# Kernel optimization log

Hardware: AMD Instinct MI355X
Metric: run time of the kernel (lower is better)

Reference implementation:

```python
import jax, jax.numpy as jnp
import numpy as np

I, H, O = 3, 16, 5
B, S = 4096, 512


def setup_inputs() -> dict:
    key = jax.random.key(0)
    ks = jax.random.split(key, 4)
    scale = 0.1  # xavier gain=0.1 ballpark; exact init irrelevant for correctness baseline
    return {
        "x": jax.random.normal(ks[0], (B, S, I), dtype=jnp.float32),
        "W_ih": jax.random.normal(ks[1], (4 * H, I), dtype=jnp.float32) * scale,
        "W_hh": jax.random.normal(ks[2], (4 * H, H), dtype=jnp.float32) * scale,
        "b_ih": jnp.zeros((4 * H,), dtype=jnp.float32),
        "b_hh": jnp.zeros((4 * H,), dtype=jnp.float32),
        "W_lin": jax.random.normal(ks[3], (O, H), dtype=jnp.float32) * scale,
        "b_lin": jnp.zeros((O,), dtype=jnp.float32),
    }


def _lstm(x, W_ih, W_hh, b_ih, b_hh):
    # Precompute input contribution for all timesteps: [B, S, 4H]
    xg = jnp.einsum('bsi,gi->bsg', x, W_ih) + b_ih + b_hh
    xg = jnp.swapaxes(xg, 0, 1)  # [S, B, 4H] for scan
    h0 = jnp.zeros((x.shape[0], H), dtype=x.dtype)
    c0 = jnp.zeros_like(h0)

    def step(carry, xt):
        h, c = carry
        gates = xt + h @ W_hh.T  # [B, 4H]
        i, f, g, o = jnp.split(gates, 4, axis=-1)  # PyTorch gate order i,f,g,o
        i = jax.nn.sigmoid(i)
        f = jax.nn.sigmoid(f)
        g = jnp.tanh(g)
        o = jax.nn.sigmoid(o)
        c = f * c + i * g
        h = o * jnp.tanh(c)
        return (h, c), h

    _, hs = jax.lax.scan(step, (h0, c0), xg)
    return jnp.swapaxes(hs, 0, 1)  # [B, S, H]


def reference(x, W_ih, W_hh, b_ih, b_hh, W_lin, b_lin):
    out1 = _lstm(x, W_ih, W_hh, b_ih, b_hh)            # [B, S, H]
    out = jnp.einsum('bsh,oh->bso', out1, W_lin) + b_lin  # [B, S, O]
    return jnp.clip(out, -10.0, 10.0)
```

## Files before the change

kernel.cpp:

```cpp
#include <hip/hip_runtime.h>


#define TS 512
#define LOG2E 1.44269504088896340736f

typedef float f32x2 __attribute__((ext_vector_type(2)));

#define BCAST(K) hbr[K] = __int_as_float( \
    __builtin_amdgcn_update_dpp(0, hvi, 0x150 + (K), 0xf, 0xf, true))
#define BCAST_ALL() \
  BCAST(0); BCAST(1); BCAST(2); BCAST(3); BCAST(4); BCAST(5); BCAST(6); BCAST(7); \
  BCAST(8); BCAST(9); BCAST(10); BCAST(11); BCAST(12); BCAST(13); BCAST(14); BCAST(15)

__global__ __launch_bounds__(256, 1)
void lstm_enc_kernel(const float* __restrict__ x,
                     const float* __restrict__ W_ih,
                     const float* __restrict__ W_hh,
                     const float* __restrict__ b_ih,
                     const float* __restrict__ b_hh,
                     const float* __restrict__ W_lin,
                     const float* __restrict__ b_lin,
                     float* __restrict__ out) {
  const int tid = threadIdx.x;
  const int j = tid & 15;
  const int batch = blockIdx.x * 16 + (tid >> 4);
  const int jo = (j < 5) ? j : 0;

  f32x2 wif[16], wgo[16];
  float wl[16];
#pragma unroll
  for (int k = 0; k < 16; ++k) {
    wif[k] = f32x2{W_hh[(j     ) * 16 + k] * LOG2E,
                   W_hh[(j + 16) * 16 + k] * LOG2E};
    wgo[k] = f32x2{W_hh[(j + 32) * 16 + k] * (2.0f * LOG2E),
                   W_hh[(j + 48) * 16 + k] * LOG2E};
    wl[k]  = W_lin[jo * 16 + k];
  }
  f32x2 xif[3], xgo[3];
#pragma unroll
  for (int i = 0; i < 3; ++i) {
    xif[i] = f32x2{W_ih[(j     ) * 3 + i] * LOG2E,
                   W_ih[(j + 16) * 3 + i] * LOG2E};
    xgo[i] = f32x2{W_ih[(j + 32) * 3 + i] * (2.0f * LOG2E),
                   W_ih[(j + 48) * 3 + i] * LOG2E};
  }
  const f32x2 bif = f32x2{(b_ih[j     ] + b_hh[j     ]) * LOG2E,
                          (b_ih[j + 16] + b_hh[j + 16]) * LOG2E};
  const f32x2 bgo = f32x2{(b_ih[j + 32] + b_hh[j + 32]) * (2.0f * LOG2E),
                          (b_ih[j + 48] + b_hh[j + 48]) * LOG2E};
  const float bl = b_lin[jo];

  const float* __restrict__ xb = x + (size_t)batch * (TS * 3);
  float* __restrict__ ob = out + (size_t)batch * (TS * 5) + j;

  float h = 0.0f, c = 0.0f;
  float x0 = xb[0], x1 = xb[1], x2 = xb[2];

  for (int t = 0; t < TS; ++t) {
    const int tn = (t + 1) & (TS - 1);
    const float nx0 = xb[tn * 3 + 0];
    const float nx1 = xb[tn * 3 + 1];
    const float nx2 = xb[tn * 3 + 2];

    float hbr[16];
    const int hvi = __float_as_int(h);
    BCAST_ALL();

    f32x2 aif = bif, ago = bgo;
    float oa = bl;
    aif = f32x2{x0, x0} * xif[0] + aif;
    aif = f32x2{x1, x1} * xif[1] + aif;
    aif = f32x2{x2, x2} * xif[2] + aif;
    ago = f32x2{x0, x0} * xgo[0] + ago;
    ago = f32x2{x1, x1} * xgo[1] + ago;
    ago = f32x2{x2, x2} * xgo[2] + ago;
#pragma unroll
    for (int k = 0; k < 16; ++k) {
      const float hk = hbr[k];
      const f32x2 h2 = f32x2{hk, hk};
      aif = h2 * wif[k] + aif;
      ago = h2 * wgo[k] + ago;
      oa = fmaf(hk, wl[k], oa);
    }

    if (t > 0 && j < 5) {
      ob[(t - 1) * 5] = fminf(fmaxf(oa, -10.0f), 10.0f);
    }

    const float ig = __builtin_amdgcn_rcpf(1.0f + __builtin_amdgcn_exp2f(-aif.x));
    const float fg = __builtin_amdgcn_rcpf(1.0f + __builtin_amdgcn_exp2f(-aif.y));
    const float gg = fmaf(-2.0f, __builtin_amdgcn_rcpf(1.0f + __builtin_amdgcn_exp2f(ago.x)), 1.0f);
    const float og = __builtin_amdgcn_rcpf(1.0f + __builtin_amdgcn_exp2f(-ago.y));

    c = fmaf(fg, c, ig * gg);
    const float tc = fmaf(-2.0f,
        __builtin_amdgcn_rcpf(1.0f + __builtin_amdgcn_exp2f((2.0f * LOG2E) * c)), 1.0f);
    h = og * tc;

    x0 = nx0; x1 = nx1; x2 = nx2;
  }

  {
    float hbr[16];
    const int hvi = __float_as_int(h);
    BCAST_ALL();
    float oa = bl;
#pragma unroll
    for (int k = 0; k < 16; ++k) oa = fmaf(hbr[k], wl[k], oa);
    if (j < 5) {
      ob[(TS - 1) * 5] = fminf(fmaxf(oa, -10.0f), 10.0f);
    }
  }
}

extern "C" void kernel_launch(void* const* d_in, const int* in_sizes, int n_in,
                              void* d_out, int out_size, void* d_ws, size_t ws_size,
                              hipStream_t stream) {
  const float* x     = (const float*)d_in[0];
  const float* W_ih  = (const float*)d_in[1];
  const float* W_hh  = (const float*)d_in[2];
  const float* b_ih  = (const float*)d_in[3];
  const float* b_hh  = (const float*)d_in[4];
  const float* W_lin = (const float*)d_in[5];
  const float* b_lin = (const float*)d_in[6];
  float* out = (float*)d_out;

  const int B = in_sizes[0] / (TS * 3);
  const int grid = B / 16;
  lstm_enc_kernel<<<grid, 256, 0, stream>>>(x, W_ih, W_hh, b_ih, b_hh, W_lin, b_lin, out);
}
```

Measured before the change: 236.5 us.

## Split LSTM gates across two 16-lane rows and exchange via ds_swizzle

Each batch element now uses 32 lanes instead of 16. One 16-lane row computes the i/f gates and the other the g/o gates, halving the per-lane recurrent FMA work and the transcendentals. The gate results are exchanged with a ds_swizzle, and the accumulation is split into two chains to expose ILP. The grid doubles and launch bounds allow two blocks per CU, trading more threads, redundant cell/h updates and the output dot product on both rows, plus swizzle latency, for a shorter per-step critical path.

```diff
diff --git a/kernel.cpp b/kernel.cpp
--- a/kernel.cpp
+++ b/kernel.cpp
@@ -12,7 +12,9 @@
   BCAST(0); BCAST(1); BCAST(2); BCAST(3); BCAST(4); BCAST(5); BCAST(6); BCAST(7); \
   BCAST(8); BCAST(9); BCAST(10); BCAST(11); BCAST(12); BCAST(13); BCAST(14); BCAST(15)
 
-__global__ __launch_bounds__(256, 1)
+#define SWZ16(vi) __builtin_amdgcn_ds_swizzle((vi), 0x401F)
+
+__global__ __launch_bounds__(256, 2)
 void lstm_enc_kernel(const float* __restrict__ x,
                      const float* __restrict__ W_ih,
                      const float* __restrict__ W_hh,
@@ -23,35 +25,34 @@
                      float* __restrict__ out) {
   const int tid = threadIdx.x;
   const int j = tid & 15;
-  const int batch = blockIdx.x * 16 + (tid >> 4);
+  const bool rowB = (tid & 16) != 0;
+  const int batch = blockIdx.x * 8 + (tid >> 5);
   const int jo = (j < 5) ? j : 0;
 
-  f32x2 wif[16], wgo[16];
+  const int g0 = rowB ? j + 32 : j;
+  const int g1 = rowB ? j + 48 : j + 16;
+  const float s0 = rowB ? 2.0f * LOG2E : -LOG2E;
+  const float s1 = -LOG2E;
+
+  f32x2 wz[16];
   float wl[16];
 #pragma unroll
   for (int k = 0; k < 16; ++k) {
-    wif[k] = f32x2{W_hh[(j     ) * 16 + k] * LOG2E,
-                   W_hh[(j + 16) * 16 + k] * LOG2E};
-    wgo[k] = f32x2{W_hh[(j + 32) * 16 + k] * (2.0f * LOG2E),
-                   W_hh[(j + 48) * 16 + k] * LOG2E};
-    wl[k]  = W_lin[jo * 16 + k];
+    wz[k] = f32x2{W_hh[g0 * 16 + k] * s0, W_hh[g1 * 16 + k] * s1};
+    wl[k] = W_lin[jo * 16 + k];
   }
-  f32x2 xif[3], xgo[3];
+  f32x2 xw[3];
 #pragma unroll
   for (int i = 0; i < 3; ++i) {
-    xif[i] = f32x2{W_ih[(j     ) * 3 + i] * LOG2E,
-                   W_ih[(j + 16) * 3 + i] * LOG2E};
-    xgo[i] = f32x2{W_ih[(j + 32) * 3 + i] * (2.0f * LOG2E),
-                   W_ih[(j + 48) * 3 + i] * LOG2E};
+    xw[i] = f32x2{W_ih[g0 * 3 + i] * s0, W_ih[g1 * 3 + i] * s1};
   }
-  const f32x2 bif = f32x2{(b_ih[j     ] + b_hh[j     ]) * LOG2E,
-                          (b_ih[j + 16] + b_hh[j + 16]) * LOG2E};
-  const f32x2 bgo = f32x2{(b_ih[j + 32] + b_hh[j + 32]) * (2.0f * LOG2E),
-                          (b_ih[j + 48] + b_hh[j + 48]) * LOG2E};
+  const f32x2 bz = f32x2{(b_ih[g0] + b_hh[g0]) * s0,
+                         (b_ih[g1] + b_hh[g1]) * s1};
   const float bl = b_lin[jo];
 
   const float* __restrict__ xb = x + (size_t)batch * (TS * 3);
   float* __restrict__ ob = out + (size_t)batch * (TS * 5) + j;
+  const bool storer = (tid & 31) < 5;
 
   float h = 0.0f, c = 0.0f;
   float x0 = xb[0], x1 = xb[1], x2 = xb[2];
@@ -66,32 +67,35 @@
     const int hvi = __float_as_int(h);
     BCAST_ALL();
 
-    f32x2 aif = bif, ago = bgo;
+    f32x2 za = bz, zb = f32x2{0.0f, 0.0f};
+    za = f32x2{x0, x0} * xw[0] + za;
+    zb = f32x2{x1, x1} * xw[1] + zb;
+    za = f32x2{x2, x2} * xw[2] + za;
+#pragma unroll
+    for (int k = 0; k < 16; k += 2) {
+      za = f32x2{hbr[k], hbr[k]} * wz[k] + za;
+      zb = f32x2{hbr[k + 1], hbr[k + 1]} * wz[k + 1] + zb;
+    }
+    const f32x2 z = za + zb;
+
     float oa = bl;
-    aif = f32x2{x0, x0} * xif[0] + aif;
-    aif = f32x2{x1, x1} * xif[1] + aif;
-    aif = f32x2{x2, x2} * xif[2] + aif;
-    ago = f32x2{x0, x0} * xgo[0] + ago;
-    ago = f32x2{x1, x1} * xgo[1] + ago;
-    ago = f32x2{x2, x2} * xgo[2] + ago;
 #pragma unroll
-    for (int k = 0; k < 16; ++k) {
-      const float hk = hbr[k];
-      const f32x2 h2 = f32x2{hk, hk};
-      aif = h2 * wif[k] + aif;
-      ago = h2 * wgo[k] + ago;
-      oa = fmaf(hk, wl[k], oa);
-    }
-
-    if (t > 0 && j < 5) {
+    for (int k = 0; k < 16; ++k) oa = fmaf(hbr[k], wl[k], oa);
+    if (t > 0 && storer) {
       ob[(t - 1) * 5] = fminf(fmaxf(oa, -10.0f), 10.0f);
     }
 
-    const float ig = __builtin_amdgcn_rcpf(1.0f + __builtin_amdgcn_exp2f(-aif.x));
-    const float fg = __builtin_amdgcn_rcpf(1.0f + __builtin_amdgcn_exp2f(-aif.y));
-    const float gg = fmaf(-2.0f, __builtin_amdgcn_rcpf(1.0f + __builtin_amdgcn_exp2f(ago.x)), 1.0f);
-    const float og = __builtin_amdgcn_rcpf(1.0f + __builtin_amdgcn_exp2f(-ago.y));
+    const float r0 = __builtin_amdgcn_rcpf(1.0f + __builtin_amdgcn_exp2f(z.x));
+    const float r1 = __builtin_amdgcn_rcpf(1.0f + __builtin_amdgcn_exp2f(z.y));
 
+    const float q0 = __int_as_float(SWZ16(__float_as_int(r0)));
+    const float q1 = __int_as_float(SWZ16(__float_as_int(r1)));
+    const float ig = rowB ? q0 : r0;
+    const float fg = rowB ? q1 : r1;
+    const float sg = rowB ? r0 : q0;
+    const float og = rowB ? r1 : q1;
+
+    const float gg = fmaf(-2.0f, sg, 1.0f);
     c = fmaf(fg, c, ig * gg);
     const float tc = fmaf(-2.0f,
         __builtin_amdgcn_rcpf(1.0f + __builtin_amdgcn_exp2f((2.0f * LOG2E) * c)), 1.0f);
@@ -107,7 +111,7 @@
     float oa = bl;
 #pragma unroll
     for (int k = 0; k < 16; ++k) oa = fmaf(hbr[k], wl[k], oa);
-    if (j < 5) {
+    if (storer) {
       ob[(TS - 1) * 5] = fminf(fmaxf(oa, -10.0f), 10.0f);
     }
   }
@@ -126,6 +130,6 @@
   float* out = (float*)d_out;
 
   const int B = in_sizes[0] / (TS * 3);
-  const int grid = B / 16;
+  const int grid = B / 8;
   lstm_enc_kernel<<<grid, 256, 0, stream>>>(x, W_ih, W_hh, b_ih, b_hh, W_lin, b_lin, out);
 }
```

Measured after the change: 267.1 us. 1.13x slower.

## Stage x through LDS in 64-step chunks and split gate accumulators into two chains

Applied to the files above, without the earlier changes.

The 16 lanes of each batch group now cooperatively load 64 timesteps of x with coalesced float4 loads and scatter them into a double-buffered shared-memory tile. Each step then reads its x values from LDS with a two-step lookahead instead of issuing three scalar global loads per timestep. The gate dot products are split into two independent FMA accumulator chains to shorten the dependency chain on the recurrent critical path. This adds LDS traffic and register pressure. There is no barrier between the LDS writes and the reads, which relies on the 16 lanes of a group sharing one wavefront.

```diff
diff --git a/kernel.cpp b/kernel.cpp
--- a/kernel.cpp
+++ b/kernel.cpp
@@ -23,8 +23,12 @@
                      float* __restrict__ out) {
   const int tid = threadIdx.x;
   const int j = tid & 15;
-  const int batch = blockIdx.x * 16 + (tid >> 4);
+  const int g = tid >> 4;
+  const int batch = blockIdx.x * 16 + g;
   const int jo = (j < 5) ? j : 0;
+
+  __shared__ float4 xs[2][64][16];
+  float4* xsf = &xs[0][0][0];
 
   f32x2 wif[16], wgo[16];
   float wl[16];
@@ -36,12 +40,16 @@
                    W_hh[(j + 48) * 16 + k] * LOG2E};
     wl[k]  = W_lin[jo * 16 + k];
   }
-  f32x2 xif[3], xgo[3];
+  f32x2 xw[3];
 #pragma unroll
   for (int i = 0; i < 3; ++i) {
-    xif[i] = f32x2{W_ih[(j     ) * 3 + i] * LOG2E,
-                   W_ih[(j + 16) * 3 + i] * LOG2E};
-    xgo[i] = f32x2{W_ih[(j + 32) * 3 + i] * (2.0f * LOG2E),
+    xw[i] = f32x2{W_ih[(j     ) * 3 + i] * LOG2E,
+                  W_ih[(j + 16) * 3 + i] * LOG2E};
+  }
+  f32x2 xwg[3];
+#pragma unroll
+  for (int i = 0; i < 3; ++i) {
+    xwg[i] = f32x2{W_ih[(j + 32) * 3 + i] * (2.0f * LOG2E),
                    W_ih[(j + 48) * 3 + i] * LOG2E};
   }
   const f32x2 bif = f32x2{(b_ih[j     ] + b_hh[j     ]) * LOG2E,
@@ -52,52 +60,101 @@
 
   const float* __restrict__ xb = x + (size_t)batch * (TS * 3);
   float* __restrict__ ob = out + (size_t)batch * (TS * 5) + j;
+  const bool storer = (j < 5);
+
+  const float* xc0 = xb + j * 12;
+  float4 q0, q1, q2;
+
+  q0 = *(const float4*)(xc0 + 0);
+  q1 = *(const float4*)(xc0 + 4);
+  q2 = *(const float4*)(xc0 + 8);
+  {
+    const int wb = j * 4 * 16 + g;
+    xsf[wb +  0] = float4{q0.x, q0.y, q0.z, 0.f};
+    xsf[wb + 16] = float4{q0.w, q1.x, q1.y, 0.f};
+    xsf[wb + 32] = float4{q1.z, q1.w, q2.x, 0.f};
+    xsf[wb + 48] = float4{q2.y, q2.z, q2.w, 0.f};
+  }
+  q0 = *(const float4*)(xc0 + 192 + 0);
+  q1 = *(const float4*)(xc0 + 192 + 4);
+  q2 = *(const float4*)(xc0 + 192 + 8);
+
+  float4 xr[2];
+  xr[0] = xsf[0 * 16 + g];
+  xr[1] = xsf[1 * 16 + g];
 
   float h = 0.0f, c = 0.0f;
-  float x0 = xb[0], x1 = xb[1], x2 = xb[2];
 
-  for (int t = 0; t < TS; ++t) {
-    const int tn = (t + 1) & (TS - 1);
-    const float nx0 = xb[tn * 3 + 0];
-    const float nx1 = xb[tn * 3 + 1];
-    const float nx2 = xb[tn * 3 + 2];
+  auto step = [&](int s, int slot) {
+    const float4 xt = xr[slot];
+    xr[slot] = xsf[(((s + 2) & 127) << 4) + g];
 
     float hbr[16];
     const int hvi = __float_as_int(h);
     BCAST_ALL();
 
-    f32x2 aif = bif, ago = bgo;
+    f32x2 aa = bif, ab = f32x2{0.f, 0.f};
+    f32x2 ga = bgo, gb = f32x2{0.f, 0.f};
+    aa = f32x2{xt.x, xt.x} * xw[0] + aa;
+    ab = f32x2{xt.y, xt.y} * xw[1] + ab;
+    aa = f32x2{xt.z, xt.z} * xw[2] + aa;
+    ga = f32x2{xt.x, xt.x} * xwg[0] + ga;
+    gb = f32x2{xt.y, xt.y} * xwg[1] + gb;
+    ga = f32x2{xt.z, xt.z} * xwg[2] + ga;
+#pragma unroll
+    for (int k = 0; k < 16; k += 2) {
+      const f32x2 h0 = f32x2{hbr[k], hbr[k]};
+      const f32x2 h1 = f32x2{hbr[k + 1], hbr[k + 1]};
+      aa = h0 * wif[k] + aa;
+      ab = h1 * wif[k + 1] + ab;
+      ga = h0 * wgo[k] + ga;
+      gb = h1 * wgo[k + 1] + gb;
+    }
+    const f32x2 zif = aa + ab;
+    const f32x2 zgo = ga + gb;
+
     float oa = bl;
-    aif = f32x2{x0, x0} * xif[0] + aif;
-    aif = f32x2{x1, x1} * xif[1] + aif;
-    aif = f32x2{x2, x2} * xif[2] + aif;
-    ago = f32x2{x0, x0} * xgo[0] + ago;
-    ago = f32x2{x1, x1} * xgo[1] + ago;
-    ago = f32x2{x2, x2} * xgo[2] + ago;
 #pragma unroll
-    for (int k = 0; k < 16; ++k) {
-      const float hk = hbr[k];
-      const f32x2 h2 = f32x2{hk, hk};
-      aif = h2 * wif[k] + aif;
-      ago = h2 * wgo[k] + ago;
-      oa = fmaf(hk, wl[k], oa);
+    for (int k = 0; k < 16; ++k) oa = fmaf(hbr[k], wl[k], oa);
+    if (s > 0 && storer) {
+      ob[(s - 1) * 5] = fminf(fmaxf(oa, -10.0f), 10.0f);
     }
 
-    if (t > 0 && j < 5) {
-      ob[(t - 1) * 5] = fminf(fmaxf(oa, -10.0f), 10.0f);
-    }
+    const float ig = __builtin_amdgcn_rcpf(1.0f + __builtin_amdgcn_exp2f(-zif.x));
+    const float fg = __builtin_amdgcn_rcpf(1.0f + __builtin_amdgcn_exp2f(-zif.y));
+    const float sg = __builtin_amdgcn_rcpf(1.0f + __builtin_amdgcn_exp2f(zgo.x));
+    const float og = __builtin_amdgcn_rcpf(1.0f + __builtin_amdgcn_exp2f(-zgo.y));
 
-    const float ig = __builtin_amdgcn_rcpf(1.0f + __builtin_amdgcn_exp2f(-aif.x));
-    const float fg = __builtin_amdgcn_rcpf(1.0f + __builtin_amdgcn_exp2f(-aif.y));
-    const float gg = fmaf(-2.0f, __builtin_amdgcn_rcpf(1.0f + __builtin_amdgcn_exp2f(ago.x)), 1.0f);
-    const float og = __builtin_amdgcn_rcpf(1.0f + __builtin_amdgcn_exp2f(-ago.y));
-
+    const float gg = fmaf(-2.0f, sg, 1.0f);
     c = fmaf(fg, c, ig * gg);
     const float tc = fmaf(-2.0f,
         __builtin_amdgcn_rcpf(1.0f + __builtin_amdgcn_exp2f((2.0f * LOG2E) * c)), 1.0f);
     h = og * tc;
+  };
 
-    x0 = nx0; x1 = nx1; x2 = nx2;
+  for (int ch = 0; ch < 8; ++ch) {
+    const int base = ch * 64;
+
+#pragma unroll 2
+    for (int u = 0; u < 32; ++u) step(base + u, u & 1);
+
+    if (ch < 7) {
+      const int p = (ch + 1) & 1;
+      const int wb = p * 1024 + j * 64 + g;
+      xsf[wb +  0] = float4{q0.x, q0.y, q0.z, 0.f};
+      xsf[wb + 16] = float4{q0.w, q1.x, q1.y, 0.f};
+      xsf[wb + 32] = float4{q1.z, q1.w, q2.x, 0.f};
+      xsf[wb + 48] = float4{q2.y, q2.z, q2.w, 0.f};
+    }
+    if (ch < 6) {
+      const float* xc = xc0 + (ch + 2) * 192;
+      q0 = *(const float4*)(xc + 0);
+      q1 = *(const float4*)(xc + 4);
+      q2 = *(const float4*)(xc + 8);
+    }
+
+#pragma unroll 2
+    for (int u = 32; u < 64; ++u) step(base + u, u & 1);
   }
 
   {
@@ -107,7 +164,7 @@
     float oa = bl;
 #pragma unroll
     for (int k = 0; k < 16; ++k) oa = fmaf(hbr[k], wl[k], oa);
-    if (j < 5) {
+    if (storer) {
       ob[(TS - 1) * 5] = fminf(fmaxf(oa, -10.0f), 10.0f);
     }
   }
```

New measurement: 220.1 us. 1.07x faster.
